# Optimization experiments

Hardware: AMD Instinct MI355X
Metric: run time of the kernel (lower is better)

Reference implementation:

```python
import jax, jax.numpy as jnp
import numpy as np

B, T, C = 2, 2048, 1024
NH = 16
HS = C // NH

def setup_inputs() -> dict:
    key = jax.random.key(0)
    ks = jax.random.split(key, 5)
    x = jax.random.normal(ks[0], (B, T, C), dtype=jnp.float32)
    scale = 1.0 / np.sqrt(C)
    Wk = jax.random.normal(ks[1], (C, C), dtype=jnp.float32) * scale
    bk = jax.random.normal(ks[2], (C,), dtype=jnp.float32) * scale
    Wv = jax.random.normal(ks[3], (C, C), dtype=jnp.float32) * scale
    bv = jax.random.normal(ks[4], (C,), dtype=jnp.float32) * scale
    return {"x": x, "Wk": Wk, "bk": bk, "Wv": Wv, "bv": bv}

def reference(x, Wk, bk, Wv, bv):
    b, t, c = x.shape
    # projections: key and value are Dense; query is identity (as in source)
    k = (x @ Wk + bk).reshape(b, t, NH, HS).transpose(0, 2, 1, 3)  # b nh T hs
    q = x.reshape(b, t, NH, HS).transpose(0, 2, 1, 3)              # b nh T hs
    v = (x @ Wv + bv).reshape(b, t, NH, HS).transpose(0, 2, 1, 3)  # b nh T hs
    # NOTE: source computes logits = K @ Q^T (no 1/sqrt(d) scaling)
    logits = jnp.einsum('bhid,bhjd->bhij', k, q)                   # b nh T T
    causal = jnp.tril(jnp.ones((t, t), dtype=bool))                # True where allowed
    masked = jnp.where(causal[None, None, :, :], logits, -jnp.inf)
    att = jax.nn.softmax(masked, axis=-1)
    y = jnp.einsum('bhij,bhjd->bhid', att, v)                      # b nh T hs
    return y.transpose(0, 2, 1, 3).reshape(b, t, c)
```

## Files before the change

kernel.cpp:

```cpp
#include <hip/hip_runtime.h>
#include <cstdint>
#include <cstddef>

#define BB  2
#define TT  2048
#define CC  1024
#define NHH 16
#define HSS 64
#define BT  (BB*TT)

typedef unsigned short u16;
typedef unsigned int u32;
typedef _Float16 f16;
typedef __attribute__((ext_vector_type(8))) _Float16 f16x8;
typedef __attribute__((ext_vector_type(8))) __bf16 bf16x8;
typedef __attribute__((ext_vector_type(4))) float f32x4;

__device__ __forceinline__ u16 f2bf(float f) {
    union { float f; u32 u; } x; x.f = f;
    return (u16)((x.u + 0x7fffu + ((x.u >> 16) & 1u)) >> 16);
}
__device__ __forceinline__ u16 f2h(float f) {
    union { f16 h; u16 u; } x; x.h = (f16)f;
    return x.u;
}

#define MFMA_BF(a,b,c) __builtin_amdgcn_mfma_f32_16x16x32_bf16((a),(b),(c),0,0,0)
#define MFMA_F16(a,b,c) __builtin_amdgcn_mfma_f32_16x16x32_f16((a),(b),(c),0,0,0)

__device__ __forceinline__ void gld16(const u16* g, u16* l) {
    __builtin_amdgcn_global_load_lds(
        (const __attribute__((address_space(1))) unsigned int*)g,
        (__attribute__((address_space(3))) unsigned int*)l, 16, 0, 0);
}

__global__ __launch_bounds__(256) void convert_x(
    const float* __restrict__ X, u16* __restrict__ Xf)
{
    const int idx = (blockIdx.x * 256 + threadIdx.x) * 8;
    const float4 a = *(const float4*)&X[idx];
    const float4 b = *(const float4*)&X[idx + 4];
    float v[8] = {a.x, a.y, a.z, a.w, b.x, b.y, b.z, b.w};
    union { uint4 u; u16 s[8]; } H;
    #pragma unroll
    for (int u = 0; u < 8; ++u) H.s[u] = f2h(v[u]);
    *(uint4*)&Xf[idx] = H.u;
}

__global__ __launch_bounds__(256) void convert_w(
    const float* __restrict__ Wk, const float* __restrict__ Wv,
    u16* __restrict__ WkT, u16* __restrict__ WvT)
{
    const bool isK = (blockIdx.z == 0);
    const float* W = isK ? Wk : Wv;
    u16* WT = isK ? WkT : WvT;
    __shared__ __align__(16) u16 LH[64][72];
    const int tid = threadIdx.x;
    const int k0 = blockIdx.y * 64, n0 = blockIdx.x * 64;
    {
        const int row = tid >> 2, coff = (tid & 3) * 16;
        const float* g = &W[(size_t)(k0 + row) * CC + n0 + coff];
        #pragma unroll
        for (int u = 0; u < 16; ++u) LH[row][coff + u] = f2h(g[u]);
    }
    __syncthreads();
    {
        const int n = tid >> 2, kc = (tid & 3) * 16;
        union { uint4 u[2]; u16 s[16]; } Hq;
        #pragma unroll
        for (int u = 0; u < 16; ++u) Hq.s[u] = LH[kc + u][n];
        uint4* ph = (uint4*)&WT[(size_t)(n0 + n) * CC + k0 + kc];
        ph[0] = Hq.u[0]; ph[1] = Hq.u[1];
    }
}

__global__ __launch_bounds__(256) void proj_kernel(
    const u16* __restrict__ Xf, const u16* __restrict__ WkT,
    const u16* __restrict__ WvT,
    const float* __restrict__ bk, const float* __restrict__ bv,
    u16* __restrict__ Kf, u16* __restrict__ Vt)
{
    __shared__ u16 SM[4][8192];

    const int id = blockIdx.x;
    const int xcd = id & 7, idx = id >> 3;
    const int z = idx >> 5, rem = idx & 31;
    const int n0 = (rem & 7) * 128;
    const int m0 = (xcd * 4 + (rem >> 3)) * 128;
    const bool isK = (z == 0);
    const u16* WT = isK ? WkT : WvT;

    const int tid = threadIdx.x;
    const int w = tid >> 6, lane = tid & 63;
    const int quad = lane >> 4, l15 = lane & 15;
    const int wm = (w >> 1) * 64, wn = (w & 1) * 64;

    const u16* src = (w < 2) ? Xf : WT;
    const int rb = (w < 2) ? m0 : n0;
    int srow[8], scg[8];
    #pragma unroll
    for (int t = 0; t < 8; ++t) {
        int ci = (w & 1) * 512 + t * 64 + lane;
        srow[t] = ci >> 3;
        scg[t] = ((ci & 7) - srow[t]) & 7;
    }
    const int sbase = (w & 1) * 4096;

    f32x4 acc[4][4] = {};

    {
        u16* dst = ((w < 2) ? SM[0] : SM[2]) + sbase;
        #pragma unroll
        for (int t = 0; t < 8; ++t)
            gld16(src + (size_t)(rb + srow[t]) * CC + scg[t] * 8, dst + t * 512);
    }

    for (int ki = 0; ki < 16; ++ki) {
        const int buf = ki & 1;
        __syncthreads();
        if (ki < 15) {
            u16* dst = ((w < 2) ? SM[buf ^ 1] : SM[2 + (buf ^ 1)]) + sbase;
            const int k0n = (ki + 1) * 64;
            #pragma unroll
            for (int t = 0; t < 8; ++t)
                gld16(src + (size_t)(rb + srow[t]) * CC + k0n + scg[t] * 8,
                      dst + t * 512);
        }
        const u16* Ab = SM[buf];
        const u16* Bb = SM[2 + buf];
        #pragma unroll
        for (int kk = 0; kk < 2; ++kk) {
            f16x8 ah[4];
            #pragma unroll
            for (int i = 0; i < 4; ++i) {
                const int row = wm + i * 16 + l15;
                const int cp = ((kk * 4 + quad + row) & 7) * 8;
                ah[i] = *(const f16x8*)&Ab[row * 64 + cp];
            }
            #pragma unroll
            for (int j = 0; j < 4; ++j) {
                const int rowb = wn + j * 16 + l15;
                const int cpb = ((kk * 4 + quad + rowb) & 7) * 8;
                f16x8 bh_ = *(const f16x8*)&Bb[rowb * 64 + cpb];
                #pragma unroll
                for (int i = 0; i < 4; ++i)
                    acc[i][j] = MFMA_F16(ah[i], bh_, acc[i][j]);
            }
        }
    }

    __syncthreads();
    u16* XL = &SM[0][0];

    if (isK) {
        #pragma unroll
        for (int j = 0; j < 4; ++j) {
            const float bias = bk[n0 + wn + j * 16 + l15];
            #pragma unroll
            for (int i = 0; i < 4; ++i)
                #pragma unroll
                for (int r = 0; r < 4; ++r)
                    XL[(wm + i * 16 + quad * 4 + r) * 136 + wn + j * 16 + l15] =
                        f2h(acc[i][j][r] + bias);
        }
        __syncthreads();
        const int r = tid >> 1, half = tid & 1;
        #pragma unroll
        for (int t = 0; t < 8; ++t)
            *(uint4*)&Kf[(size_t)(m0 + r) * CC + n0 + half * 64 + t * 8] =
                *(const uint4*)&XL[r * 136 + half * 64 + t * 8];
    } else {
        #pragma unroll
        for (int j = 0; j < 4; ++j) {
            const float bias = bv[n0 + wn + j * 16 + l15];
            #pragma unroll
            for (int i = 0; i < 4; ++i) {
                uint2 pk;
                pk.x = (u32)f2bf(acc[i][j][0] + bias) |
                       ((u32)f2bf(acc[i][j][1] + bias) << 16);
                pk.y = (u32)f2bf(acc[i][j][2] + bias) |
                       ((u32)f2bf(acc[i][j][3] + bias) << 16);
                *(uint2*)&XL[(wn + j * 16 + l15) * 136 + wm + i * 16 + quad * 4] = pk;
            }
        }
        __syncthreads();
        const int nl = tid >> 1, half = tid & 1;
        const int d = (n0 + nl) & (HSS - 1), hh = (n0 + nl) >> 6;
        const int bb = m0 >> 11, tb = (m0 & (TT - 1)) + half * 64;
        const size_t gb = ((size_t)(bb * NHH + hh) * HSS + d) * TT + tb;
        #pragma unroll
        for (int t = 0; t < 8; ++t)
            *(uint4*)&Vt[gb + t * 8] = *(const uint4*)&XL[nl * 136 + half * 64 + t * 8];
    }
}

__global__ __launch_bounds__(256) void attn_kernel(
    const u16* __restrict__ Xf, const u16* __restrict__ Kf,
    const u16* __restrict__ Vt, float* __restrict__ out)
{
    __shared__ u16 Xs[2][4096];
    __shared__ u16 Vs[2][4096];
    __shared__ __align__(16) u16 Ps[4][2][1152];

    const int L = blockIdx.x;
    const int xcd = L & 7, k = (L >> 3) & 15, grp = L >> 7;
    const int hb = xcd + 8 * grp;
    const int h = hb & (NHH - 1), b = hb >> 4;
    const int iA = k, iB = 31 - k;
    const int i0A = iA * 64, i0B = iB * 64;

    const int tid = threadIdx.x;
    const int w = tid >> 6, lane = tid & 63;
    const int quad = lane >> 4, l15 = lane & 15;
    const size_t rowbase = (size_t)b * TT;
    const int hd = h * HSS;
    const size_t vgbase = (size_t)(b * NHH + h) * HSS * TT;

    bf16x8 ones;
    { union { u32 u[4]; bf16x8 v; } o;
      #pragma unroll
      for (int i = 0; i < 4; ++i) o.u[i] = 0x3F803F80u;
      ones = o.v; }

    f16x8 qA[2], qB[2];
    #pragma unroll
    for (int c = 0; c < 2; ++c) {
        qA[c] = *(const f16x8*)&Kf[(rowbase + i0A + w * 16 + l15) * CC + hd + c * 32 + quad * 8];
        qB[c] = *(const f16x8*)&Kf[(rowbase + i0B + w * 16 + l15) * CC + hd + c * 32 + quad * 8];
    }

    int crow[2], ccg[2], cbase[2];
    #pragma unroll
    for (int t = 0; t < 2; ++t) {
        const int ci = t * 256 + tid;
        crow[t] = ci >> 3;
        ccg[t] = ((ci & 7) - crow[t]) & 7;
        cbase[t] = (t * 256 + w * 64) * 8;
    }
    const u16* gx[2]; const u16* gv[2];
    #pragma unroll
    for (int t = 0; t < 2; ++t) {
        gx[t] = Xf + (rowbase + crow[t]) * CC + hd + ccg[t] * 8;
        gv[t] = Vt + vgbase + (size_t)crow[t] * TT + ccg[t] * 8;
    }

    #pragma unroll
    for (int t = 0; t < 2; ++t) {
        gld16(gx[t], Xs[0] + cbase[t]);
        gld16(gv[t], Vs[0] + cbase[t]);
    }

    f32x4 oA[4] = {}, oB[4] = {};
    f32x4 laA = {}, laB = {};

    for (int jt = 0; jt <= iB; ++jt) {
        const int buf = jt & 1;
        __syncthreads();
        if (jt < iB) {
            const int j0n = (jt + 1) * 64;
            #pragma unroll
            for (int t = 0; t < 2; ++t) {
                gld16(gx[t] + (size_t)j0n * CC, Xs[buf ^ 1] + cbase[t]);
                gld16(gv[t] + j0n, Vs[buf ^ 1] + cbase[t]);
            }
        }
        const bool doA = (jt <= iA);

        f32x4 sB[4], sA[4];
        #pragma unroll
        for (int nt = 0; nt < 4; ++nt) {
            const int krow = nt * 16 + l15;
            f16x8 x0 = *(const f16x8*)&Xs[buf][krow * 64 + ((quad + krow) & 7) * 8];
            f16x8 x1 = *(const f16x8*)&Xs[buf][krow * 64 + ((quad + 4 + krow) & 7) * 8];
            f32x4 z = {};
            z = MFMA_F16(qB[0], x0, z);
            z = MFMA_F16(qB[1], x1, z);
            sB[nt] = z;
            if (doA) {
                f32x4 y = {};
                y = MFMA_F16(qA[0], x0, y);
                y = MFMA_F16(qA[1], x1, y);
                sA[nt] = y;
            }
        }
        if (jt == iB) {
            #pragma unroll
            for (int nt = 0; nt < 4; ++nt) {
                const int jg = nt * 16 + l15;
                #pragma unroll
                for (int r = 0; r < 4; ++r)
                    if (jg > w * 16 + quad * 4 + r) sB[nt][r] = -1e30f;
            }
        }
        if (doA && jt == iA) {
            #pragma unroll
            for (int nt = 0; nt < 4; ++nt) {
                const int jg = nt * 16 + l15;
                #pragma unroll
                for (int r = 0; r < 4; ++r)
                    if (jg > w * 16 + quad * 4 + r) sA[nt][r] = -1e30f;
            }
        }

        #pragma unroll
        for (int nt = 0; nt < 4; ++nt)
            #pragma unroll
            for (int r = 0; r < 4; ++r)
                Ps[w][0][(quad * 4 + r) * 72 + nt * 16 + l15] =
                    f2bf(__expf(sB[nt][r] - 20.f));
        if (doA) {
            #pragma unroll
            for (int nt = 0; nt < 4; ++nt)
                #pragma unroll
                for (int r = 0; r < 4; ++r)
                    Ps[w][1][(quad * 4 + r) * 72 + nt * 16 + l15] =
                        f2bf(__expf(sA[nt][r] - 20.f));
        }

        bf16x8 aB0 = *(const bf16x8*)&Ps[w][0][l15 * 72 + quad * 8];
        bf16x8 aB1 = *(const bf16x8*)&Ps[w][0][l15 * 72 + 32 + quad * 8];
        laB = MFMA_BF(aB0, ones, laB);
        laB = MFMA_BF(aB1, ones, laB);
        bf16x8 aA0, aA1;
        if (doA) {
            aA0 = *(const bf16x8*)&Ps[w][1][l15 * 72 + quad * 8];
            aA1 = *(const bf16x8*)&Ps[w][1][l15 * 72 + 32 + quad * 8];
            laA = MFMA_BF(aA0, ones, laA);
            laA = MFMA_BF(aA1, ones, laA);
        }

        #pragma unroll
        for (int dt = 0; dt < 4; ++dt) {
            const int vrow = dt * 16 + l15;
            bf16x8 v0 = *(const bf16x8*)&Vs[buf][vrow * 64 + ((quad + vrow) & 7) * 8];
            bf16x8 v1 = *(const bf16x8*)&Vs[buf][vrow * 64 + ((quad + 4 + vrow) & 7) * 8];
            oB[dt] = MFMA_BF(aB0, v0, oB[dt]);
            oB[dt] = MFMA_BF(aB1, v1, oB[dt]);
            if (doA) {
                oA[dt] = MFMA_BF(aA0, v0, oA[dt]);
                oA[dt] = MFMA_BF(aA1, v1, oA[dt]);
            }
        }
    }

    float liA[4], liB[4];
    #pragma unroll
    for (int r = 0; r < 4; ++r) { liA[r] = 1.f / laA[r]; liB[r] = 1.f / laB[r]; }
    #pragma unroll
    for (int dt = 0; dt < 4; ++dt) {
        #pragma unroll
        for (int r = 0; r < 4; ++r) {
            const int igA = i0A + w * 16 + quad * 4 + r;
            const int igB = i0B + w * 16 + quad * 4 + r;
            out[(rowbase + igA) * CC + hd + dt * 16 + l15] = oA[dt][r] * liA[r];
            out[(rowbase + igB) * CC + hd + dt * 16 + l15] = oB[dt][r] * liB[r];
        }
    }
}

extern "C" void kernel_launch(void* const* d_in, const int* in_sizes, int n_in,
                              void* d_out, int out_size, void* d_ws, size_t ws_size,
                              hipStream_t stream) {
    (void)in_sizes; (void)n_in; (void)out_size; (void)ws_size;
    const float* x  = (const float*)d_in[0];
    const float* Wk = (const float*)d_in[1];
    const float* bk = (const float*)d_in[2];
    const float* Wv = (const float*)d_in[3];
    const float* bv = (const float*)d_in[4];
    float* out = (float*)d_out;

    const size_t M4 = (size_t)BT * CC;
    const size_t M1 = (size_t)CC * CC;
    u16* Xf  = (u16*)d_ws;
    u16* Kf  = Xf + M4;
    u16* Vt  = Kf + M4;
    u16* WkT = Vt + M4;
    u16* WvT = WkT + M1;

    convert_x<<<dim3(M4 / (256 * 8)), 256, 0, stream>>>(x, Xf);
    convert_w<<<dim3(16, 16, 2), 256, 0, stream>>>(Wk, Wv, WkT, WvT);
    proj_kernel<<<dim3(512), 256, 0, stream>>>(Xf, WkT, WvT, bk, bv, Kf, Vt);
    attn_kernel<<<dim3(512), 256, 0, stream>>>(Xf, Kf, Vt, out);
}
```

Before: 155.2 us.

## Keep attention probabilities in registers via transposed scores and permlane swaps

The attention loop now computes transposed score tiles (X·K instead of K·X), so each lane already holds a full row of probabilities. The LDS round-trip through the Ps buffer is replaced by packed bf16 conversion and permlane16_swap, and the V-tile read pattern is permuted to match. The log2(e) factor is folded into the K projection epilogue so exp2f is used with a constant bias in the accumulator init. Both the projection and attention loops are unrolled by two with precomputed LDS base pointers, so buffer offsets become constants. This removes per-iteration LDS writes and reads plus address arithmetic, at the cost of more register pressure and a softmax that relies on a fixed offset rather than a running max.

```diff
diff --git a/kernel.cpp b/kernel.cpp
--- a/kernel.cpp
+++ b/kernel.cpp
@@ -9,8 +9,12 @@
 #define HSS 64
 #define BT  (BB*TT)
 
+#define LOG2E 1.44269504088896f
+#define S0INIT (-28.8539008f)
+
 typedef unsigned short u16;
 typedef unsigned int u32;
+typedef __attribute__((ext_vector_type(2))) unsigned int u32x2;
 typedef _Float16 f16;
 typedef __attribute__((ext_vector_type(8))) _Float16 f16x8;
 typedef __attribute__((ext_vector_type(8))) __bf16 bf16x8;
@@ -23,6 +27,11 @@
 __device__ __forceinline__ u16 f2h(float f) {
     union { f16 h; u16 u; } x; x.h = (f16)f;
     return x.u;
+}
+__device__ __forceinline__ u32 cvtpk_bf16(float lo, float hi) {
+    u32 r;
+    asm("v_cvt_pk_bf16_f32 %0, %1, %2" : "=v"(r) : "v"(lo), "v"(hi));
+    return r;
 }
 
 #define MFMA_BF(a,b,c) __builtin_amdgcn_mfma_f32_16x16x32_bf16((a),(b),(c),0,0,0)
@@ -80,7 +89,7 @@
     const float* __restrict__ bk, const float* __restrict__ bv,
     u16* __restrict__ Kf, u16* __restrict__ Vt)
 {
-    __shared__ u16 SM[4][8192];
+    __shared__ __align__(16) u16 SM[4][8192];
 
     const int id = blockIdx.x;
     const int xcd = id & 7, idx = id >> 3;
@@ -106,6 +115,15 @@
     }
     const int sbase = (w & 1) * 4096;
 
+    const char* smA0 = (const char*)&SM[0][0] + (wm + l15) * 128 +
+                       ((quad + wm + l15) & 7) * 16;
+    const char* smA1 = (const char*)&SM[0][0] + (wm + l15) * 128 +
+                       ((4 + quad + wm + l15) & 7) * 16;
+    const char* smB0 = (const char*)&SM[0][0] + 32768 + (wn + l15) * 128 +
+                       ((quad + wn + l15) & 7) * 16;
+    const char* smB1 = (const char*)&SM[0][0] + 32768 + (wn + l15) * 128 +
+                       ((4 + quad + wn + l15) & 7) * 16;
+
     f32x4 acc[4][4] = {};
 
     {
@@ -115,39 +133,40 @@
             gld16(src + (size_t)(rb + srow[t]) * CC + scg[t] * 8, dst + t * 512);
     }
 
-    for (int ki = 0; ki < 16; ++ki) {
-        const int buf = ki & 1;
-        __syncthreads();
-        if (ki < 15) {
-            u16* dst = ((w < 2) ? SM[buf ^ 1] : SM[2 + (buf ^ 1)]) + sbase;
-            const int k0n = (ki + 1) * 64;
-            #pragma unroll
-            for (int t = 0; t < 8; ++t)
-                gld16(src + (size_t)(rb + srow[t]) * CC + k0n + scg[t] * 8,
-                      dst + t * 512);
-        }
-        const u16* Ab = SM[buf];
-        const u16* Bb = SM[2 + buf];
-        #pragma unroll
-        for (int kk = 0; kk < 2; ++kk) {
-            f16x8 ah[4];
-            #pragma unroll
-            for (int i = 0; i < 4; ++i) {
-                const int row = wm + i * 16 + l15;
-                const int cp = ((kk * 4 + quad + row) & 7) * 8;
-                ah[i] = *(const f16x8*)&Ab[row * 64 + cp];
-            }
-            #pragma unroll
-            for (int j = 0; j < 4; ++j) {
-                const int rowb = wn + j * 16 + l15;
-                const int cpb = ((kk * 4 + quad + rowb) & 7) * 8;
-                f16x8 bh_ = *(const f16x8*)&Bb[rowb * 64 + cpb];
-                #pragma unroll
-                for (int i = 0; i < 4; ++i)
-                    acc[i][j] = MFMA_F16(ah[i], bh_, acc[i][j]);
-            }
-        }
-    }
+#define PROJ_STEP(KI, BUF)                                                    \
+    {                                                                         \
+        __syncthreads();                                                      \
+        if ((KI) < 15) {                                                      \
+            u16* dst = ((w < 2) ? SM[(BUF) ^ 1] : SM[2 + ((BUF) ^ 1)]) + sbase;\
+            const int k0n = ((KI) + 1) * 64;                                  \
+            _Pragma("unroll")                                                 \
+            for (int t = 0; t < 8; ++t)                                       \
+                gld16(src + (size_t)(rb + srow[t]) * CC + k0n + scg[t] * 8,   \
+                      dst + t * 512);                                         \
+        }                                                                     \
+        _Pragma("unroll")                                                     \
+        for (int kk = 0; kk < 2; ++kk) {                                      \
+            const char* pa = kk ? smA1 : smA0;                                \
+            const char* pb = kk ? smB1 : smB0;                                \
+            f16x8 ah[4];                                                      \
+            _Pragma("unroll")                                                 \
+            for (int i = 0; i < 4; ++i)                                       \
+                ah[i] = *(const f16x8*)(pa + (BUF) * 16384 + i * 2048);       \
+            _Pragma("unroll")                                                 \
+            for (int j = 0; j < 4; ++j) {                                     \
+                f16x8 bh_ = *(const f16x8*)(pb + (BUF) * 16384 + j * 2048);   \
+                _Pragma("unroll")                                             \
+                for (int i = 0; i < 4; ++i)                                   \
+                    acc[i][j] = MFMA_F16(ah[i], bh_, acc[i][j]);              \
+            }                                                                 \
+        }                                                                     \
+    }
+
+    for (int ki = 0; ki < 16; ki += 2) {
+        PROJ_STEP(ki, 0);
+        PROJ_STEP(ki + 1, 1);
+    }
+#undef PROJ_STEP
 
     __syncthreads();
     u16* XL = &SM[0][0];
@@ -161,7 +180,7 @@
                 #pragma unroll
                 for (int r = 0; r < 4; ++r)
                     XL[(wm + i * 16 + quad * 4 + r) * 136 + wn + j * 16 + l15] =
-                        f2h(acc[i][j][r] + bias);
+                        f2h((acc[i][j][r] + bias) * LOG2E);
         }
         __syncthreads();
         const int r = tid >> 1, half = tid & 1;
@@ -198,9 +217,8 @@
     const u16* __restrict__ Xf, const u16* __restrict__ Kf,
     const u16* __restrict__ Vt, float* __restrict__ out)
 {
-    __shared__ u16 Xs[2][4096];
-    __shared__ u16 Vs[2][4096];
-    __shared__ __align__(16) u16 Ps[4][2][1152];
+    __shared__ __align__(16) u16 Xs[2][4096];
+    __shared__ __align__(16) u16 Vs[2][4096];
 
     const int L = blockIdx.x;
     const int xcd = L & 7, k = (L >> 3) & 15, grp = L >> 7;
@@ -212,6 +230,7 @@
     const int tid = threadIdx.x;
     const int w = tid >> 6, lane = tid & 63;
     const int quad = lane >> 4, l15 = lane & 15;
+    const int pq = ((quad & 1) << 1) | (quad >> 1);
     const size_t rowbase = (size_t)b * TT;
     const int hd = h * HSS;
     const size_t vgbase = (size_t)(b * NHH + h) * HSS * TT;
@@ -229,6 +248,11 @@
         qB[c] = *(const f16x8*)&Kf[(rowbase + i0B + w * 16 + l15) * CC + hd + c * 32 + quad * 8];
     }
 
+    const char* xs0 = (const char*)&Xs[0][0] + l15 * 128 + ((quad + l15) & 7) * 16;
+    const char* xs1 = (const char*)&Xs[0][0] + l15 * 128 + ((quad + 4 + l15) & 7) * 16;
+    const char* vs0 = (const char*)&Vs[0][0] + l15 * 128 + ((pq + l15) & 7) * 16;
+    const char* vs1 = (const char*)&Vs[0][0] + l15 * 128 + ((pq + 4 + l15) & 7) * 16;
+
     int crow[2], ccg[2], cbase[2];
     #pragma unroll
     for (int t = 0; t < 2; ++t) {
@@ -253,95 +277,119 @@
     f32x4 oA[4] = {}, oB[4] = {};
     f32x4 laA = {}, laB = {};
 
-    for (int jt = 0; jt <= iB; ++jt) {
-        const int buf = jt & 1;
-        __syncthreads();
-        if (jt < iB) {
-            const int j0n = (jt + 1) * 64;
-            #pragma unroll
-            for (int t = 0; t < 2; ++t) {
-                gld16(gx[t] + (size_t)j0n * CC, Xs[buf ^ 1] + cbase[t]);
-                gld16(gv[t] + j0n, Vs[buf ^ 1] + cbase[t]);
-            }
-        }
-        const bool doA = (jt <= iA);
-
-        f32x4 sB[4], sA[4];
-        #pragma unroll
-        for (int nt = 0; nt < 4; ++nt) {
-            const int krow = nt * 16 + l15;
-            f16x8 x0 = *(const f16x8*)&Xs[buf][krow * 64 + ((quad + krow) & 7) * 8];
-            f16x8 x1 = *(const f16x8*)&Xs[buf][krow * 64 + ((quad + 4 + krow) & 7) * 8];
-            f32x4 z = {};
-            z = MFMA_F16(qB[0], x0, z);
-            z = MFMA_F16(qB[1], x1, z);
-            sB[nt] = z;
-            if (doA) {
-                f32x4 y = {};
-                y = MFMA_F16(qA[0], x0, y);
-                y = MFMA_F16(qA[1], x1, y);
-                sA[nt] = y;
-            }
-        }
-        if (jt == iB) {
-            #pragma unroll
-            for (int nt = 0; nt < 4; ++nt) {
-                const int jg = nt * 16 + l15;
-                #pragma unroll
-                for (int r = 0; r < 4; ++r)
-                    if (jg > w * 16 + quad * 4 + r) sB[nt][r] = -1e30f;
-            }
-        }
-        if (doA && jt == iA) {
-            #pragma unroll
-            for (int nt = 0; nt < 4; ++nt) {
-                const int jg = nt * 16 + l15;
-                #pragma unroll
-                for (int r = 0; r < 4; ++r)
-                    if (jg > w * 16 + quad * 4 + r) sA[nt][r] = -1e30f;
-            }
-        }
-
-        #pragma unroll
-        for (int nt = 0; nt < 4; ++nt)
-            #pragma unroll
-            for (int r = 0; r < 4; ++r)
-                Ps[w][0][(quad * 4 + r) * 72 + nt * 16 + l15] =
-                    f2bf(__expf(sB[nt][r] - 20.f));
-        if (doA) {
-            #pragma unroll
-            for (int nt = 0; nt < 4; ++nt)
-                #pragma unroll
-                for (int r = 0; r < 4; ++r)
-                    Ps[w][1][(quad * 4 + r) * 72 + nt * 16 + l15] =
-                        f2bf(__expf(sA[nt][r] - 20.f));
-        }
-
-        bf16x8 aB0 = *(const bf16x8*)&Ps[w][0][l15 * 72 + quad * 8];
-        bf16x8 aB1 = *(const bf16x8*)&Ps[w][0][l15 * 72 + 32 + quad * 8];
-        laB = MFMA_BF(aB0, ones, laB);
-        laB = MFMA_BF(aB1, ones, laB);
-        bf16x8 aA0, aA1;
-        if (doA) {
-            aA0 = *(const bf16x8*)&Ps[w][1][l15 * 72 + quad * 8];
-            aA1 = *(const bf16x8*)&Ps[w][1][l15 * 72 + 32 + quad * 8];
-            laA = MFMA_BF(aA0, ones, laA);
-            laA = MFMA_BF(aA1, ones, laA);
-        }
-
-        #pragma unroll
-        for (int dt = 0; dt < 4; ++dt) {
-            const int vrow = dt * 16 + l15;
-            bf16x8 v0 = *(const bf16x8*)&Vs[buf][vrow * 64 + ((quad + vrow) & 7) * 8];
-            bf16x8 v1 = *(const bf16x8*)&Vs[buf][vrow * 64 + ((quad + 4 + vrow) & 7) * 8];
-            oB[dt] = MFMA_BF(aB0, v0, oB[dt]);
-            oB[dt] = MFMA_BF(aB1, v1, oB[dt]);
-            if (doA) {
-                oA[dt] = MFMA_BF(aA0, v0, oA[dt]);
-                oA[dt] = MFMA_BF(aA1, v1, oA[dt]);
-            }
-        }
-    }
+#define ATTN_BODY(JT, BUF)                                                    \
+    {                                                                         \
+        __syncthreads();                                                      \
+        if ((JT) + 1 <= iB) {                                                 \
+            const int j0n = ((JT) + 1) * 64;                                  \
+            _Pragma("unroll")                                                 \
+            for (int t = 0; t < 2; ++t) {                                     \
+                gld16(gx[t] + (size_t)j0n * CC, Xs[(BUF) ^ 1] + cbase[t]);    \
+                gld16(gv[t] + j0n, Vs[(BUF) ^ 1] + cbase[t]);                 \
+            }                                                                 \
+        }                                                                     \
+        const bool doA_ = (JT) <= iA;                                         \
+        f32x4 sB[4], sA[4];                                                   \
+        _Pragma("unroll")                                                     \
+        for (int nt = 0; nt < 4; ++nt) {                                      \
+            f16x8 x0 = *(const f16x8*)(xs0 + (BUF) * 8192 + nt * 2048);       \
+            f16x8 x1 = *(const f16x8*)(xs1 + (BUF) * 8192 + nt * 2048);       \
+            f32x4 z = {S0INIT, S0INIT, S0INIT, S0INIT};                       \
+            z = MFMA_F16(x0, qB[0], z);                                       \
+            z = MFMA_F16(x1, qB[1], z);                                       \
+            sB[nt] = z;                                                       \
+            if (doA_) {                                                       \
+                f32x4 y = {S0INIT, S0INIT, S0INIT, S0INIT};                   \
+                y = MFMA_F16(x0, qA[0], y);                                   \
+                y = MFMA_F16(x1, qA[1], y);                                   \
+                sA[nt] = y;                                                   \
+            }                                                                 \
+        }                                                                     \
+        if ((JT) == iB) {                                                     \
+            _Pragma("unroll")                                                 \
+            for (int nt = 0; nt < 4; ++nt)                                    \
+                _Pragma("unroll")                                             \
+                for (int r = 0; r < 4; ++r)                                   \
+                    if (nt * 16 + quad * 4 + r > w * 16 + l15)                \
+                        sB[nt][r] = -1e30f;                                   \
+        }                                                                     \
+        if (doA_ && (JT) == iA) {                                             \
+            _Pragma("unroll")                                                 \
+            for (int nt = 0; nt < 4; ++nt)                                    \
+                _Pragma("unroll")                                             \
+                for (int r = 0; r < 4; ++r)                                   \
+                    if (nt * 16 + quad * 4 + r > w * 16 + l15)                \
+                        sA[nt][r] = -1e30f;                                   \
+        }                                                                     \
+        u32 pB_[4][2];                                                        \
+        _Pragma("unroll")                                                     \
+        for (int nt = 0; nt < 4; ++nt) {                                      \
+            pB_[nt][0] = cvtpk_bf16(exp2f(sB[nt][0]), exp2f(sB[nt][1]));      \
+            pB_[nt][1] = cvtpk_bf16(exp2f(sB[nt][2]), exp2f(sB[nt][3]));      \
+        }                                                                     \
+        _Pragma("unroll")                                                     \
+        for (int c = 0; c < 2; ++c)                                           \
+            _Pragma("unroll")                                                 \
+            for (int p = 0; p < 2; ++p) {                                     \
+                u32x2 sw = __builtin_amdgcn_permlane16_swap(                  \
+                    pB_[2 * c][p], pB_[2 * c + 1][p], false, false);          \
+                pB_[2 * c][p] = sw[0];                                        \
+                pB_[2 * c + 1][p] = sw[1];                                    \
+            }                                                                 \
+        union { u32 u[4]; bf16x8 v; } ub0, ub1;                               \
+        ub0.u[0] = pB_[0][0]; ub0.u[1] = pB_[0][1];                           \
+        ub0.u[2] = pB_[1][0]; ub0.u[3] = pB_[1][1];                           \
+        ub1.u[0] = pB_[2][0]; ub1.u[1] = pB_[2][1];                           \
+        ub1.u[2] = pB_[3][0]; ub1.u[3] = pB_[3][1];                           \
+        bf16x8 aB0 = ub0.v, aB1 = ub1.v;                                      \
+        bf16x8 aA0, aA1;                                                      \
+        if (doA_) {                                                           \
+            u32 pA_[4][2];                                                    \
+            _Pragma("unroll")                                                 \
+            for (int nt = 0; nt < 4; ++nt) {                                  \
+                pA_[nt][0] = cvtpk_bf16(exp2f(sA[nt][0]), exp2f(sA[nt][1]));  \
+                pA_[nt][1] = cvtpk_bf16(exp2f(sA[nt][2]), exp2f(sA[nt][3]));  \
+            }                                                                 \
+            _Pragma("unroll")                                                 \
+            for (int c = 0; c < 2; ++c)                                       \
+                _Pragma("unroll")                                             \
+                for (int p = 0; p < 2; ++p) {                                 \
+                    u32x2 sw = __builtin_amdgcn_permlane16_swap(              \
+                        pA_[2 * c][p], pA_[2 * c + 1][p], false, false);      \
+                    pA_[2 * c][p] = sw[0];                                    \
+                    pA_[2 * c + 1][p] = sw[1];                                \
+                }                                                             \
+            union { u32 u[4]; bf16x8 v; } ua0, ua1;                           \
+            ua0.u[0] = pA_[0][0]; ua0.u[1] = pA_[0][1];                       \
+            ua0.u[2] = pA_[1][0]; ua0.u[3] = pA_[1][1];                       \
+            ua1.u[0] = pA_[2][0]; ua1.u[1] = pA_[2][1];                       \
+            ua1.u[2] = pA_[3][0]; ua1.u[3] = pA_[3][1];                       \
+            aA0 = ua0.v; aA1 = ua1.v;                                         \
+        }                                                                     \
+        laB = MFMA_BF(aB0, ones, laB);                                        \
+        laB = MFMA_BF(aB1, ones, laB);                                        \
+        if (doA_) {                                                           \
+            laA = MFMA_BF(aA0, ones, laA);                                    \
+            laA = MFMA_BF(aA1, ones, laA);                                    \
+        }                                                                     \
+        _Pragma("unroll")                                                     \
+        for (int dt = 0; dt < 4; ++dt) {                                      \
+            bf16x8 v0 = *(const bf16x8*)(vs0 + (BUF) * 8192 + dt * 2048);     \
+            bf16x8 v1 = *(const bf16x8*)(vs1 + (BUF) * 8192 + dt * 2048);     \
+            oB[dt] = MFMA_BF(aB0, v0, oB[dt]);                                \
+            oB[dt] = MFMA_BF(aB1, v1, oB[dt]);                                \
+            if (doA_) {                                                       \
+                oA[dt] = MFMA_BF(aA0, v0, oA[dt]);                            \
+                oA[dt] = MFMA_BF(aA1, v1, oA[dt]);                            \
+            }                                                                 \
+        }                                                                     \
+    }
+
+    for (int jt = 0; jt <= iB; jt += 2) {
+        ATTN_BODY(jt, 0);
+        if (jt + 1 <= iB) ATTN_BODY(jt + 1, 1);
+    }
+#undef ATTN_BODY
 
     float liA[4], liB[4];
     #pragma unroll
```

New measurement: 153.9 us. No clear change (-0.8%).
